# Optimization experiments

Measured on AMD Instinct MI355X. Metric: run time of the kernel, lower is better.

Reference implementation:

```python
import jax, jax.numpy as jnp
import numpy as np

B, I, L = 128, 32, 96   # batch, input_dim, time_series_length
H = 512                  # hidden_dim
F = 24                   # forecast_length (t_eval points)
S = 16                   # n_samples


def _lin(k, out_dim, in_dim):
    kw, kb = jax.random.split(k)
    bound = 1.0 / np.sqrt(in_dim)
    W = jax.random.uniform(kw, (out_dim, in_dim), jnp.float32, -bound, bound)
    b = jax.random.uniform(kb, (out_dim,), jnp.float32, -bound, bound)
    return W, b


def setup_inputs() -> dict:
    key = jax.random.key(0)
    ks = jax.random.split(key, 12)
    enc_Wih, enc_bih = _lin(ks[0], 3 * H, I)
    enc_Whh, enc_bhh = _lin(ks[1], 3 * H, H)
    f_W1, f_b1 = _lin(ks[2], H, H)
    f_W2, f_b2 = _lin(ks[3], H, H)
    g_W, g_b = _lin(ks[4], H, H)
    dec_Wih, dec_bih = _lin(ks[5], 3 * H, H)
    dec_Whh, dec_bhh = _lin(ks[6], 3 * H, H)
    out_W, out_b = _lin(ks[7], I, H)
    x = jax.random.normal(ks[8], (B, I, L), jnp.float32)
    noise = jax.random.normal(ks[9], (S, F - 1, B, H), jnp.float32)  # unit normals -> dW = sqrt(dt)*noise
    return dict(x=x, noise=noise,
                enc_Wih=enc_Wih, enc_Whh=enc_Whh, enc_bih=enc_bih, enc_bhh=enc_bhh,
                f_W1=f_W1, f_b1=f_b1, f_W2=f_W2, f_b2=f_b2,
                g_W=g_W, g_b=g_b,
                dec_Wih=dec_Wih, dec_Whh=dec_Whh, dec_bih=dec_bih, dec_bhh=dec_bhh,
                out_W=out_W, out_b=out_b)


def _gru_cell(gi, gh, h):
    ir, iz, inn = jnp.split(gi, 3, axis=-1)
    hr, hz, hn = jnp.split(gh, 3, axis=-1)
    r = jax.nn.sigmoid(ir + hr)
    z = jax.nn.sigmoid(iz + hz)
    n = jnp.tanh(inn + r * hn)
    return (1.0 - z) * n + z * h


def reference(x, noise, enc_Wih, enc_Whh, enc_bih, enc_bhh,
              f_W1, f_b1, f_W2, f_b2, g_W, g_b,
              dec_Wih, dec_Whh, dec_bih, dec_bhh, out_W, out_b):
    Bb, Ii = x.shape[0], x.shape[1]
    Ss, steps = noise.shape[0], noise.shape[1]
    Hh = enc_Whh.shape[1]
    Ff = steps + 1  # forecast_length; t_eval=linspace(0,F,F) -> F-1 euler steps

    # ---- encoder GRU over [B, L, I] (x permuted from [B, I, L]) ----
    xs = jnp.transpose(x, (0, 2, 1))  # [B, L, I]
    gi_all = jnp.einsum('bli,gi->lbg', xs, enc_Wih) + enc_bih  # [L, B, 3H]

    def enc_step(h, gi):
        gh = h @ enc_Whh.T + enc_bhh
        return _gru_cell(gi, gh, h), None

    h0 = jnp.zeros((Bb, Hh), x.dtype)
    h_enc, _ = jax.lax.scan(enc_step, h0, gi_all)  # [B, H]

    # ---- Euler-Maruyama SDE integration, samples merged into batch ----
    dt = Ff / steps  # linspace(0, F, F): dt = F/(F-1)
    sqdt = jnp.sqrt(jnp.asarray(dt, x.dtype))
    h_sde = jnp.broadcast_to(h_enc, (Ss, Bb, Hh)).reshape(Ss * Bb, Hh)
    dW = (noise * sqdt).transpose(1, 0, 2, 3).reshape(steps, Ss * Bb, Hh)

    def sde_step(h, dw):
        f = jnp.tanh(h @ f_W1.T + f_b1) @ f_W2.T + f_b2
        g = jax.nn.softplus(h @ g_W.T + g_b)
        return h + f * dt + g * dw, None

    h_T, _ = jax.lax.scan(sde_step, h_sde, dW)  # [S*B, H]

    # ---- decoder GRU with zero inputs (input proj reduces to bias) ----
    gi0 = dec_bih  # W_ih @ 0 + b_ih

    def dec_step(h, _):
        gh = h @ dec_Whh.T + dec_bhh
        h_new = _gru_cell(gi0, gh, h)
        return h_new, h_new

    _, hs = jax.lax.scan(dec_step, h_T, None, length=Ff)  # [F, S*B, H]

    out = hs @ out_W.T + out_b          # [F, S*B, I]
    out = out.transpose(1, 2, 0)        # [S*B, I, F]
    return out.reshape(Ss, Bb, Ii, Ff)  # [S, B, I, F]
```

## Files before the change

### kernel.cpp

```cpp
#include <hip/hip_runtime.h>
#include <math.h>

typedef __bf16 bf16x8 __attribute__((ext_vector_type(8)));
typedef float f32x4 __attribute__((ext_vector_type(4)));
typedef unsigned long long u64;

#define HD 512
#define NB 128
#define NI 32
#define NL 96
#define NS 16
#define NF 24
#define NSTEP 23
#define PAD 520

#define MFMA16(a,b,c) __builtin_amdgcn_mfma_f32_16x16x32_bf16(a,b,c,0,0,0)

__device__ __forceinline__ unsigned short f2bf(float f) {
    union { float f; unsigned u; } v; v.f = f;
    unsigned r = v.u + 0x7fffu + ((v.u >> 16) & 1u);
    return (unsigned short)(r >> 16);
}
__device__ __forceinline__ float bf2f(unsigned short h) {
    union { unsigned u; float f; } v; v.u = ((unsigned)h) << 16;
    return v.f;
}
__device__ __forceinline__ void split_bf(float v, unsigned short& hi, unsigned short& lo) {
    unsigned short h = f2bf(v);
    hi = h;
    lo = f2bf(v - bf2f(h));
}
__device__ __forceinline__ float sigm(float x) { return 1.0f / (1.0f + __expf(-x)); }
__device__ __forceinline__ float softp(float x) {
    return fmaxf(x, 0.0f) + log1pf(__expf(-fabsf(x)));
}
__device__ __forceinline__ bf16x8 ld8(const unsigned short* p) {
    return *reinterpret_cast<const bf16x8*>(p);
}
__device__ __forceinline__ f32x4 mfma3(bf16x8 ahi, bf16x8 alo, const unsigned short* bp, f32x4 c) {
    bf16x8 bhi = ld8(bp);
    bf16x8 blo = ld8(bp + 8);
    c = MFMA16(ahi, bhi, c);
    c = MFMA16(alo, bhi, c);
    c = MFMA16(ahi, blo, c);
    return c;
}

__device__ __forceinline__ void sigval(unsigned* slot, unsigned val, int tid) {
    __builtin_amdgcn_s_waitcnt(0);
    __syncthreads();
    if (tid == 0)
        __hip_atomic_store(slot, val, __ATOMIC_RELAXED, __HIP_MEMORY_SCOPE_AGENT);
}
__device__ __forceinline__ void poll8(const unsigned* f, unsigned tgt, int wv, int lane) {
    if (wv == 0) {
        for (;;) {
            unsigned v = __hip_atomic_load(f + (lane & 7), __ATOMIC_RELAXED, __HIP_MEMORY_SCOPE_AGENT);
            if (__all((int)(v >= tgt))) break;
            __builtin_amdgcn_s_sleep(2);
        }
    }
    __syncthreads();
}
__device__ __forceinline__ void stage64(const u64* sh, const u64* sl, int r0,
        unsigned short (*Ahi)[16][PAD], unsigned short (*Alo)[16][PAD], int tid) {
    #pragma unroll 1
    for (int c = 0; c < 4; ++c) {
        u64 th[4], tl[4];
        #pragma unroll
        for (int k = 0; k < 4; ++k) {
            int idx = (c * 4 + k) * 512 + tid;
            int r = idx >> 7, c4 = idx & 127;
            th[k] = __hip_atomic_load(sh + (size_t)(r0 + r) * 128 + c4,
                                      __ATOMIC_RELAXED, __HIP_MEMORY_SCOPE_AGENT);
            tl[k] = __hip_atomic_load(sl + (size_t)(r0 + r) * 128 + c4,
                                      __ATOMIC_RELAXED, __HIP_MEMORY_SCOPE_AGENT);
        }
        #pragma unroll
        for (int k = 0; k < 4; ++k) {
            int idx = (c * 4 + k) * 512 + tid;
            int r = idx >> 7, c4 = idx & 127;
            *(u64*)&Ahi[r >> 4][r & 15][c4 * 4] = th[k];
            *(u64*)&Alo[r >> 4][r & 15][c4 * 4] = tl[k];
        }
    }
}
__device__ __forceinline__ void publish64(u64* dh, u64* dl, int r0, int u0c,
        unsigned short (*Bhi)[72], unsigned short (*Blo)[72], int tid) {
    #pragma unroll
    for (int rep = 0; rep < 4; ++rep) {
        int idx = rep * 512 + tid;
        int pl = idx >> 10, e = idx & 1023;
        int r = e >> 4, c = e & 15;
        u64 q = pl ? *(const u64*)&Blo[r][c * 4] : *(const u64*)&Bhi[r][c * 4];
        u64* dst = (pl ? dl : dh) + (size_t)(r0 + r) * 128 + u0c + c;
        __hip_atomic_store(dst, q, __ATOMIC_RELAXED, __HIP_MEMORY_SCOPE_AGENT);
    }
}

__global__ void pack_w(const float* __restrict__ W, unsigned short* __restrict__ Wp,
                       int N, int K) {
    int idx = blockIdx.x * 256 + threadIdx.x;
    int total = (N / 16) * (K / 32) * 64;
    if (idx >= total) return;
    int lane = idx & 63;
    int t2 = idx >> 6;
    int KT = K / 32;
    int kt = t2 % KT, nt = t2 / KT;
    const float* src = W + (size_t)(nt * 16 + (lane & 15)) * K + kt * 32 + (lane >> 4) * 8;
    unsigned short* dst = Wp + (size_t)idx * 16;
    #pragma unroll
    for (int j = 0; j < 8; ++j) split_bf(src[j], dst[j], dst[8 + j]);
}

__global__ void pack_x(const float* __restrict__ x, unsigned short* __restrict__ xhi,
                       unsigned short* __restrict__ xlo) {
    int idx = blockIdx.x * 256 + threadIdx.x;
    if (idx >= NL * NB) return;
    int b = idx % NB, l = idx / NB;
    size_t base = (size_t)(l * NB + b) * NI;
    #pragma unroll
    for (int i = 0; i < NI; ++i)
        split_bf(x[((size_t)b * NI + i) * NL + l], xhi[base + i], xlo[base + i]);
}

__global__ __launch_bounds__(512, 2) void coop_all(
    const unsigned short* __restrict__ xhi, const unsigned short* __restrict__ xlo,
    const unsigned short* __restrict__ wih_p, const unsigned short* __restrict__ whh_p,
    const unsigned short* __restrict__ w1_p, const unsigned short* __restrict__ w2_p,
    const unsigned short* __restrict__ gw_p, const unsigned short* __restrict__ dwhh_p,
    const unsigned short* __restrict__ outw_p,
    const float* __restrict__ ebih, const float* __restrict__ ebhh,
    const float* __restrict__ fb1, const float* __restrict__ fb2,
    const float* __restrict__ gb, const float* __restrict__ dbih,
    const float* __restrict__ dbhh, const float* __restrict__ outb,
    const float* __restrict__ noise,
    u64* hS0h, u64* hS0l, u64* hS1h, u64* hS1l,
    u64* uPh, u64* uPl, u64* hD0h, u64* hD0l, u64* hD1h, u64* hD1l,
    float* out, unsigned* bar)
{
    const int bid = blockIdx.x;
    const int tid = threadIdx.x, lane = tid & 63, wv = tid >> 6;
    const int l15 = lane & 15, g4 = lane >> 4;
    const f32x4 zz = {0.f, 0.f, 0.f, 0.f};

    __shared__ __align__(16) unsigned char SM[151552];
    auto hA64hi = reinterpret_cast<unsigned short (*)[16][PAD]>(SM);
    auto hA64lo = reinterpret_cast<unsigned short (*)[16][PAD]>(SM + 66560);
    auto uShi   = reinterpret_cast<unsigned short (*)[72]>(SM + 133120);
    auto uSlo   = reinterpret_cast<unsigned short (*)[72]>(SM + 142336);
    auto pred   = reinterpret_cast<float (*)[8][16][16]>(SM);
    auto ehAhi  = reinterpret_cast<unsigned short (*)[PAD]>(SM + 32768);
    auto ehAlo  = reinterpret_cast<unsigned short (*)[PAD]>(SM + 49408);
    auto Shi    = reinterpret_cast<unsigned short (*)[16]>(SM + 66048);
    auto Slo    = reinterpret_cast<unsigned short (*)[16]>(SM + 66560);

    u64* bufh[2] = {hS0h, hS1h};
    u64* bufl[2] = {hS0l, hS1l};

    {
        const int m = bid >> 5, n = bid & 31;
        unsigned* fl = bar + m * 32;
        float cr = 0.f, cz = 0.f, binx = 0.f, bhnn = 0.f, hcell = 0.f;
        const int crow = tid >> 4, cunit = tid & 15;
        if (tid < 256) {
            int u = n * 16 + cunit;
            cr = ebih[u] + ebhh[u];
            cz = ebih[HD + u] + ebhh[HD + u];
            binx = ebih[2 * HD + u];
            bhnn = ebhh[2 * HD + u];
        }
        #pragma unroll 1
        for (int l = 0; l < NL; ++l) {
            bf16x8 axh, axl;
            if (wv == 0) {
                size_t xb = ((size_t)l * NB + m * 16 + l15) * NI + g4 * 8;
                axh = ld8(xhi + xb);
                axl = ld8(xlo + xb);
            }
            if (l > 0) {
                if (wv == 0) {
                    for (;;) {
                        unsigned v = __hip_atomic_load(fl + (lane & 31),
                                     __ATOMIC_RELAXED, __HIP_MEMORY_SCOPE_AGENT);
                        if (__all((int)(v >= (unsigned)l))) break;
                        __builtin_amdgcn_s_sleep(2);
                    }
                }
                __syncthreads();
            }
            {
                const u64* sh = bufh[l & 1];
                const u64* sl = bufl[l & 1];
                u64 qh[4], ql[4];
                #pragma unroll
                for (int rep = 0; rep < 4; ++rep) {
                    int idx = rep * 512 + tid;
                    int r = idx >> 7, c4 = idx & 127;
                    qh[rep] = __hip_atomic_load(sh + (size_t)(m * 16 + r) * 128 + c4,
                                                __ATOMIC_RELAXED, __HIP_MEMORY_SCOPE_AGENT);
                    ql[rep] = __hip_atomic_load(sl + (size_t)(m * 16 + r) * 128 + c4,
                                                __ATOMIC_RELAXED, __HIP_MEMORY_SCOPE_AGENT);
                }
                #pragma unroll
                for (int rep = 0; rep < 4; ++rep) {
                    int idx = rep * 512 + tid;
                    int r = idx >> 7, c4 = idx & 127;
                    *(u64*)&ehAhi[r][c4 * 4] = qh[rep];
                    *(u64*)&ehAlo[r][c4 * 4] = ql[rep];
                }
            }
            __syncthreads();
            f32x4 pr = zz, pz = zz, pnh = zz, pnx = zz;
            if (wv == 0) {
                pr  = mfma3(axh, axl, wih_p + ((size_t)(0 * 32 + n) * 64 + lane) * 16, pr);
                pz  = mfma3(axh, axl, wih_p + ((size_t)(1 * 32 + n) * 64 + lane) * 16, pz);
                pnx = mfma3(axh, axl, wih_p + ((size_t)(2 * 32 + n) * 64 + lane) * 16, pnx);
            }
            #pragma unroll
            for (int kk = 0; kk < 2; ++kk) {
                int kt = wv * 2 + kk;
                bf16x8 ah = *(const bf16x8*)&ehAhi[l15][kt * 32 + g4 * 8];
                bf16x8 al = *(const bf16x8*)&ehAlo[l15][kt * 32 + g4 * 8];
                pr  = mfma3(ah, al, whh_p + ((size_t)((0 * 32 + n) * 16 + kt) * 64 + lane) * 16, pr);
                pz  = mfma3(ah, al, whh_p + ((size_t)((1 * 32 + n) * 16 + kt) * 64 + lane) * 16, pz);
                pnh = mfma3(ah, al, whh_p + ((size_t)((2 * 32 + n) * 16 + kt) * 64 + lane) * 16, pnh);
            }
            #pragma unroll
            for (int v = 0; v < 4; ++v) {
                pred[0][wv][g4 * 4 + v][l15] = pr[v];
                pred[1][wv][g4 * 4 + v][l15] = pz[v];
                pred[2][wv][g4 * 4 + v][l15] = pnh[v];
                if (wv == 0) pred[3][0][g4 * 4 + v][l15] = pnx[v];
            }
            __syncthreads();
            if (tid < 256) {
                float ar = 0.f, az = 0.f, anh_ = 0.f;
                #pragma unroll
                for (int w = 0; w < 8; ++w) {
                    ar += pred[0][w][crow][cunit];
                    az += pred[1][w][crow][cunit];
                    anh_ += pred[2][w][crow][cunit];
                }
                float anx_ = pred[3][0][crow][cunit];
                float r = sigm(ar + cr);
                float z = sigm(az + cz);
                float nn = tanhf(anx_ + binx + r * (anh_ + bhnn));
                hcell = (1.f - z) * nn + z * hcell;
                unsigned short hi, lo;
                split_bf(hcell, hi, lo);
                Shi[crow][cunit] = hi;
                Slo[crow][cunit] = lo;
            }
            __syncthreads();
            if (tid < 128) {
                int p = tid >> 6, t = tid & 63;
                int r = t >> 2, c4 = t & 3;
                u64 q = p ? *(const u64*)&Slo[r][c4 * 4] : *(const u64*)&Shi[r][c4 * 4];
                u64* dst = p ? bufl[(l + 1) & 1] : bufh[(l + 1) & 1];
                __hip_atomic_store(dst + (size_t)(m * 16 + r) * 128 + n * 4 + c4, q,
                                   __ATOMIC_RELAXED, __HIP_MEMORY_SCOPE_AGENT);
            }
            __builtin_amdgcn_s_waitcnt(0);
            __syncthreads();
            if (tid == 0)
                __hip_atomic_store(fl + n, (unsigned)(l + 1),
                                   __ATOMIC_RELAXED, __HIP_MEMORY_SCOPE_AGENT);
        }
        if (tid == 0)
            __hip_atomic_fetch_add(bar + 256, 1u, __ATOMIC_RELAXED, __HIP_MEMORY_SCOPE_AGENT);
    }

    if (tid == 0) {
        while (__hip_atomic_load(bar + 256, __ATOMIC_RELAXED, __HIP_MEMORY_SCOPE_AGENT) < 256u)
            __builtin_amdgcn_s_sleep(2);
    }
    __syncthreads();

    const int m2 = bid >> 3, n2 = bid & 7;
    const int rt = wv & 3, nc = wv >> 2;
    const int r0g = m2 * 64;
    const int u0 = n2 * 64, u0c = n2 * 16;
    const int s = m2 >> 1, b0 = (m2 & 1) * 64;
    unsigned* uf = bar + 320 + m2 * 8;
    unsigned* hf = bar + 576 + m2 * 8;
    u64* hDh[2] = {hD0h, hD1h};
    u64* hDl[2] = {hD0l, hD1l};

    stage64(hS0h, hS0l, b0, hA64hi, hA64lo, tid);
    __syncthreads();

    float hreg[2][4];
    #pragma unroll
    for (int nt = 0; nt < 2; ++nt)
        #pragma unroll
        for (int v = 0; v < 4; ++v) {
            int cc = u0 + nc * 32 + nt * 16 + l15;
            hreg[nt][v] = bf2f(hA64hi[rt][g4 * 4 + v][cc]) + bf2f(hA64lo[rt][g4 * 4 + v][cc]);
        }

    float b1v[2], b2v[2], gbv[2];
    #pragma unroll
    for (int nt = 0; nt < 2; ++nt) {
        int u = u0 + nc * 32 + nt * 16 + l15;
        b1v[nt] = fb1[u]; b2v[nt] = fb2[u]; gbv[nt] = gb[u];
    }
    const float dt = (float)NF / (float)NSTEP;
    const float sqdt = sqrtf(dt);

    #pragma unroll 1
    for (int st = 0; st < NSTEP; ++st) {
        f32x4 au[2] = {zz, zz}, ag[2] = {zz, zz};
        #pragma unroll 2
        for (int kt = 0; kt < 16; ++kt) {
            bf16x8 ah = *(const bf16x8*)&hA64hi[rt][l15][kt * 32 + g4 * 8];
            bf16x8 al = *(const bf16x8*)&hA64lo[rt][l15][kt * 32 + g4 * 8];
            #pragma unroll
            for (int nt = 0; nt < 2; ++nt) {
                int ntg = n2 * 4 + nc * 2 + nt;
                au[nt] = mfma3(ah, al, w1_p + ((size_t)(ntg * 16 + kt) * 64 + lane) * 16, au[nt]);
                ag[nt] = mfma3(ah, al, gw_p + ((size_t)(ntg * 16 + kt) * 64 + lane) * 16, ag[nt]);
            }
        }
        float nz[2][4];
        #pragma unroll
        for (int nt = 0; nt < 2; ++nt)
            #pragma unroll
            for (int v = 0; v < 4; ++v)
                nz[nt][v] = noise[((size_t)(s * NSTEP + st) * NB + b0 + rt * 16 + g4 * 4 + v) * HD
                                  + u0 + nc * 32 + nt * 16 + l15];
        #pragma unroll
        for (int nt = 0; nt < 2; ++nt)
            #pragma unroll
            for (int v = 0; v < 4; ++v) {
                unsigned short hi, lo;
                split_bf(tanhf(au[nt][v] + b1v[nt]), hi, lo);
                uShi[rt * 16 + g4 * 4 + v][nc * 32 + nt * 16 + l15] = hi;
                uSlo[rt * 16 + g4 * 4 + v][nc * 32 + nt * 16 + l15] = lo;
            }
        __syncthreads();
        publish64(uPh, uPl, r0g, u0c, uShi, uSlo, tid);
        sigval(uf + n2, (unsigned)(st + 1), tid);
        poll8(uf, (unsigned)(st + 1), wv, lane);
        stage64(uPh, uPl, r0g, hA64hi, hA64lo, tid);
        __syncthreads();
        f32x4 af[2] = {zz, zz};
        #pragma unroll 2
        for (int kt = 0; kt < 16; ++kt) {
            bf16x8 uh = *(const bf16x8*)&hA64hi[rt][l15][kt * 32 + g4 * 8];
            bf16x8 ul = *(const bf16x8*)&hA64lo[rt][l15][kt * 32 + g4 * 8];
            #pragma unroll
            for (int nt = 0; nt < 2; ++nt) {
                int ntg = n2 * 4 + nc * 2 + nt;
                af[nt] = mfma3(uh, ul, w2_p + ((size_t)(ntg * 16 + kt) * 64 + lane) * 16, af[nt]);
            }
        }
        #pragma unroll
        for (int nt = 0; nt < 2; ++nt)
            #pragma unroll
            for (int v = 0; v < 4; ++v) {
                float gg = softp(ag[nt][v] + gbv[nt]);
                hreg[nt][v] += (af[nt][v] + b2v[nt]) * dt + gg * sqdt * nz[nt][v];
                unsigned short hi, lo;
                split_bf(hreg[nt][v], hi, lo);
                uShi[rt * 16 + g4 * 4 + v][nc * 32 + nt * 16 + l15] = hi;
                uSlo[rt * 16 + g4 * 4 + v][nc * 32 + nt * 16 + l15] = lo;
            }
        __syncthreads();
        publish64(hDh[(st + 1) & 1], hDl[(st + 1) & 1], r0g, u0c, uShi, uSlo, tid);
        sigval(hf + n2, (unsigned)(st + 1), tid);
        poll8(hf, (unsigned)(st + 1), wv, lane);
        stage64(hDh[(st + 1) & 1], hDl[(st + 1) & 1], r0g, hA64hi, hA64lo, tid);
        __syncthreads();
    }

    float crv[2], czv[2], binv[2], bhnv[2];
    #pragma unroll
    for (int nt = 0; nt < 2; ++nt) {
        int u = u0 + nc * 32 + nt * 16 + l15;
        crv[nt] = dbih[u] + dbhh[u];
        czv[nt] = dbih[HD + u] + dbhh[HD + u];
        binv[nt] = dbih[2 * HD + u];
        bhnv[nt] = dbhh[2 * HD + u];
    }
    float obias[2] = {0.f, 0.f};
    if (n2 == 0 && wv < 4) {
        obias[0] = outb[l15];
        obias[1] = outb[16 + l15];
    }

    #pragma unroll 1
    for (int j = 0; j <= NF; ++j) {
        if (j >= 1 && n2 == 0 && wv < 4) {
            f32x4 ao[2] = {zz, zz};
            #pragma unroll 2
            for (int kt = 0; kt < 16; ++kt) {
                bf16x8 ah = *(const bf16x8*)&hA64hi[rt][l15][kt * 32 + g4 * 8];
                bf16x8 al = *(const bf16x8*)&hA64lo[rt][l15][kt * 32 + g4 * 8];
                #pragma unroll
                for (int nt = 0; nt < 2; ++nt)
                    ao[nt] = mfma3(ah, al, outw_p + ((size_t)(nt * 16 + kt) * 64 + lane) * 16, ao[nt]);
            }
            #pragma unroll
            for (int nt = 0; nt < 2; ++nt)
                #pragma unroll
                for (int v = 0; v < 4; ++v) {
                    int b = b0 + rt * 16 + g4 * 4 + v;
                    out[(((size_t)s * NB + b) * NI + nt * 16 + l15) * NF + (j - 1)]
                        = ao[nt][v] + obias[nt];
                }
        }
        if (j == NF) break;
        f32x4 ar[2] = {zz, zz}, az[2] = {zz, zz}, anh[2] = {zz, zz};
        #pragma unroll 2
        for (int kt = 0; kt < 16; ++kt) {
            bf16x8 ah = *(const bf16x8*)&hA64hi[rt][l15][kt * 32 + g4 * 8];
            bf16x8 al = *(const bf16x8*)&hA64lo[rt][l15][kt * 32 + g4 * 8];
            #pragma unroll
            for (int nt = 0; nt < 2; ++nt) {
                int ntg = n2 * 4 + nc * 2 + nt;
                ar[nt]  = mfma3(ah, al, dwhh_p + ((size_t)((ntg) * 16 + kt) * 64 + lane) * 16, ar[nt]);
                az[nt]  = mfma3(ah, al, dwhh_p + ((size_t)((32 + ntg) * 16 + kt) * 64 + lane) * 16, az[nt]);
                anh[nt] = mfma3(ah, al, dwhh_p + ((size_t)((64 + ntg) * 16 + kt) * 64 + lane) * 16, anh[nt]);
            }
        }
        #pragma unroll
        for (int nt = 0; nt < 2; ++nt)
            #pragma unroll
            for (int v = 0; v < 4; ++v) {
                float r = sigm(ar[nt][v] + crv[nt]);
                float z = sigm(az[nt][v] + czv[nt]);
                float nn2 = tanhf(binv[nt] + r * (anh[nt][v] + bhnv[nt]));
                hreg[nt][v] = (1.f - z) * nn2 + z * hreg[nt][v];
                unsigned short hi, lo;
                split_bf(hreg[nt][v], hi, lo);
                uShi[rt * 16 + g4 * 4 + v][nc * 32 + nt * 16 + l15] = hi;
                uSlo[rt * 16 + g4 * 4 + v][nc * 32 + nt * 16 + l15] = lo;
            }
        __syncthreads();
        publish64(hDh[(NSTEP + j + 1) & 1], hDl[(NSTEP + j + 1) & 1], r0g, u0c, uShi, uSlo, tid);
        sigval(hf + n2, (unsigned)(NSTEP + j + 1), tid);
        poll8(hf, (unsigned)(NSTEP + j + 1), wv, lane);
        stage64(hDh[(NSTEP + j + 1) & 1], hDl[(NSTEP + j + 1) & 1], r0g, hA64hi, hA64lo, tid);
        __syncthreads();
    }
}

extern "C" void kernel_launch(void* const* d_in, const int* in_sizes, int n_in,
                              void* d_out, int out_size, void* d_ws, size_t ws_size,
                              hipStream_t stream) {
    const float* x       = (const float*)d_in[0];
    const float* noise   = (const float*)d_in[1];
    const float* enc_Wih = (const float*)d_in[2];
    const float* enc_Whh = (const float*)d_in[3];
    const float* enc_bih = (const float*)d_in[4];
    const float* enc_bhh = (const float*)d_in[5];
    const float* f_W1    = (const float*)d_in[6];
    const float* f_b1    = (const float*)d_in[7];
    const float* f_W2    = (const float*)d_in[8];
    const float* f_b2    = (const float*)d_in[9];
    const float* g_W     = (const float*)d_in[10];
    const float* g_b     = (const float*)d_in[11];
    const float* dec_Whh = (const float*)d_in[13];
    const float* dec_bih = (const float*)d_in[14];
    const float* dec_bhh = (const float*)d_in[15];
    const float* out_W   = (const float*)d_in[16];
    const float* out_b   = (const float*)d_in[17];
    float* out = (float*)d_out;

    char* ws = (char*)d_ws;
    unsigned short* whh_p  = (unsigned short*)(ws + 0);
    unsigned short* wih_p  = (unsigned short*)(ws + 3145728);
    unsigned short* w1_p   = (unsigned short*)(ws + 3342336);
    unsigned short* w2_p   = (unsigned short*)(ws + 4390912);
    unsigned short* gw_p   = (unsigned short*)(ws + 5439488);
    unsigned short* dwhh_p = (unsigned short*)(ws + 6488064);
    unsigned short* outw_p = (unsigned short*)(ws + 9633792);
    unsigned short* xhi    = (unsigned short*)(ws + 9699328);
    unsigned short* xlo    = (unsigned short*)(ws + 10485760);
    u64*            hS0h   = (u64*)(ws + 11272192);
    u64*            hS0l   = (u64*)(ws + 11403264);
    u64*            hS1h   = (u64*)(ws + 11534336);
    u64*            hS1l   = (u64*)(ws + 11665408);
    unsigned*       bar    = (unsigned*)(ws + 11796480);
    u64*            uPh    = (u64*)(ws + 11800576);
    u64*            uPl    = (u64*)(ws + 13897728);
    u64*            hD0h   = (u64*)(ws + 15994880);
    u64*            hD0l   = (u64*)(ws + 18092032);
    u64*            hD1h   = (u64*)(ws + 20189184);
    u64*            hD1l   = (u64*)(ws + 22286336);

    hipMemsetAsync(ws + 11272192, 0, 262144, stream);
    hipMemsetAsync(ws + 11796480, 0, 4096, stream);

    pack_w<<<384, 256, 0, stream>>>(enc_Whh, whh_p, 3 * HD, HD);
    pack_w<<<24, 256, 0, stream>>>(enc_Wih, wih_p, 3 * HD, NI);
    pack_w<<<128, 256, 0, stream>>>(f_W1, w1_p, HD, HD);
    pack_w<<<128, 256, 0, stream>>>(f_W2, w2_p, HD, HD);
    pack_w<<<128, 256, 0, stream>>>(g_W, gw_p, HD, HD);
    pack_w<<<384, 256, 0, stream>>>(dec_Whh, dwhh_p, 3 * HD, HD);
    pack_w<<<8, 256, 0, stream>>>(out_W, outw_p, NI, HD);
    pack_x<<<48, 256, 0, stream>>>(x, xhi, xlo);

    void* args[] = {
        (void*)&xhi, (void*)&xlo, (void*)&wih_p, (void*)&whh_p,
        (void*)&w1_p, (void*)&w2_p, (void*)&gw_p, (void*)&dwhh_p, (void*)&outw_p,
        (void*)&enc_bih, (void*)&enc_bhh, (void*)&f_b1, (void*)&f_b2,
        (void*)&g_b, (void*)&dec_bih, (void*)&dec_bhh, (void*)&out_b,
        (void*)&noise,
        (void*)&hS0h, (void*)&hS0l, (void*)&hS1h, (void*)&hS1l,
        (void*)&uPh, (void*)&uPl, (void*)&hD0h, (void*)&hD0l, (void*)&hD1h, (void*)&hD1l,
        (void*)&out, (void*)&bar
    };
    hipLaunchCooperativeKernel((void*)coop_all, dim3(256), dim3(512), args, 0, stream);
}
```

Before: 1.862 ms.

## Retile SDE/decoder phases to 32-row x 128-unit blocks with 16-byte coherent loads

Changes the per-block tile in the SDE and decoder phases from 64 rows x 64 units to 32 rows x 128 units. Each group of 4 blocks now synchronises instead of 8, and each block stages half as many hidden-state rows, so it also needs less LDS. Global staging loads move from 8-byte atomic loads to inline-asm dwordx4 loads with sc0 sc1 cache bypass, followed by an explicit vmcnt wait. This is meant to cut cross-block traffic and per-step synchronisation cost. The trade-offs are more weight reads per block and a reliance on asm cache bits for coherence.

```diff
diff --git a/kernel.cpp b/kernel.cpp
--- a/kernel.cpp
+++ b/kernel.cpp
@@ -3,6 +3,7 @@
 
 typedef __bf16 bf16x8 __attribute__((ext_vector_type(8)));
 typedef float f32x4 __attribute__((ext_vector_type(4)));
+typedef unsigned int u32x4 __attribute__((ext_vector_type(4)));
 typedef unsigned long long u64;
 
 #define HD 512
@@ -46,52 +47,57 @@
     return c;
 }
 
+__device__ __forceinline__ void ld16i(const void* p, u32x4& d) {
+    asm volatile("global_load_dwordx4 %0, %1, off sc0 sc1"
+                 : "=&v"(d) : "v"(p) : "memory");
+}
+__device__ __forceinline__ void ldfence() {
+    asm volatile("s_waitcnt vmcnt(0)" ::: "memory");
+    __builtin_amdgcn_sched_barrier(0);
+}
+
 __device__ __forceinline__ void sigval(unsigned* slot, unsigned val, int tid) {
     __builtin_amdgcn_s_waitcnt(0);
     __syncthreads();
     if (tid == 0)
         __hip_atomic_store(slot, val, __ATOMIC_RELAXED, __HIP_MEMORY_SCOPE_AGENT);
 }
-__device__ __forceinline__ void poll8(const unsigned* f, unsigned tgt, int wv, int lane) {
+__device__ __forceinline__ void poll4(const unsigned* f, unsigned tgt, int wv, int lane) {
     if (wv == 0) {
         for (;;) {
-            unsigned v = __hip_atomic_load(f + (lane & 7), __ATOMIC_RELAXED, __HIP_MEMORY_SCOPE_AGENT);
+            unsigned v = __hip_atomic_load(f + (lane & 3), __ATOMIC_RELAXED, __HIP_MEMORY_SCOPE_AGENT);
             if (__all((int)(v >= tgt))) break;
             __builtin_amdgcn_s_sleep(2);
         }
     }
     __syncthreads();
 }
-__device__ __forceinline__ void stage64(const u64* sh, const u64* sl, int r0,
+__device__ __forceinline__ void stage32(const u64* sh, const u64* sl, int r0,
         unsigned short (*Ahi)[16][PAD], unsigned short (*Alo)[16][PAD], int tid) {
-    #pragma unroll 1
-    for (int c = 0; c < 4; ++c) {
-        u64 th[4], tl[4];
-        #pragma unroll
-        for (int k = 0; k < 4; ++k) {
-            int idx = (c * 4 + k) * 512 + tid;
-            int r = idx >> 7, c4 = idx & 127;
-            th[k] = __hip_atomic_load(sh + (size_t)(r0 + r) * 128 + c4,
-                                      __ATOMIC_RELAXED, __HIP_MEMORY_SCOPE_AGENT);
-            tl[k] = __hip_atomic_load(sl + (size_t)(r0 + r) * 128 + c4,
-                                      __ATOMIC_RELAXED, __HIP_MEMORY_SCOPE_AGENT);
-        }
-        #pragma unroll
-        for (int k = 0; k < 4; ++k) {
-            int idx = (c * 4 + k) * 512 + tid;
-            int r = idx >> 7, c4 = idx & 127;
-            *(u64*)&Ahi[r >> 4][r & 15][c4 * 4] = th[k];
-            *(u64*)&Alo[r >> 4][r & 15][c4 * 4] = tl[k];
-        }
-    }
-}
-__device__ __forceinline__ void publish64(u64* dh, u64* dl, int r0, int u0c,
-        unsigned short (*Bhi)[72], unsigned short (*Blo)[72], int tid) {
+    u32x4 th[4], tl[4];
+    #pragma unroll
+    for (int k = 0; k < 4; ++k) {
+        int idx = k * 512 + tid;
+        int r = idx >> 6, c8 = idx & 63;
+        ld16i(sh + (size_t)(r0 + r) * 128 + c8 * 2, th[k]);
+        ld16i(sl + (size_t)(r0 + r) * 128 + c8 * 2, tl[k]);
+    }
+    ldfence();
+    #pragma unroll
+    for (int k = 0; k < 4; ++k) {
+        int idx = k * 512 + tid;
+        int r = idx >> 6, c8 = idx & 63;
+        *(u32x4*)&Ahi[r >> 4][r & 15][c8 * 8] = th[k];
+        *(u32x4*)&Alo[r >> 4][r & 15][c8 * 8] = tl[k];
+    }
+}
+__device__ __forceinline__ void publish32(u64* dh, u64* dl, int r0, int u0c,
+        unsigned short (*Bhi)[136], unsigned short (*Blo)[136], int tid) {
     #pragma unroll
     for (int rep = 0; rep < 4; ++rep) {
         int idx = rep * 512 + tid;
         int pl = idx >> 10, e = idx & 1023;
-        int r = e >> 4, c = e & 15;
+        int r = e >> 5, c = e & 31;
         u64 q = pl ? *(const u64*)&Blo[r][c * 4] : *(const u64*)&Bhi[r][c * 4];
         u64* dst = (pl ? dl : dh) + (size_t)(r0 + r) * 128 + u0c + c;
         __hip_atomic_store(dst, q, __ATOMIC_RELAXED, __HIP_MEMORY_SCOPE_AGENT);
@@ -144,11 +150,11 @@
     const int l15 = lane & 15, g4 = lane >> 4;
     const f32x4 zz = {0.f, 0.f, 0.f, 0.f};
 
-    __shared__ __align__(16) unsigned char SM[151552];
-    auto hA64hi = reinterpret_cast<unsigned short (*)[16][PAD]>(SM);
-    auto hA64lo = reinterpret_cast<unsigned short (*)[16][PAD]>(SM + 66560);
-    auto uShi   = reinterpret_cast<unsigned short (*)[72]>(SM + 133120);
-    auto uSlo   = reinterpret_cast<unsigned short (*)[72]>(SM + 142336);
+    __shared__ __align__(16) unsigned char SM[83968];
+    auto hA32hi = reinterpret_cast<unsigned short (*)[16][PAD]>(SM);
+    auto hA32lo = reinterpret_cast<unsigned short (*)[16][PAD]>(SM + 33280);
+    auto uShi   = reinterpret_cast<unsigned short (*)[136]>(SM + 66560);
+    auto uSlo   = reinterpret_cast<unsigned short (*)[136]>(SM + 75264);
     auto pred   = reinterpret_cast<float (*)[8][16][16]>(SM);
     auto ehAhi  = reinterpret_cast<unsigned short (*)[PAD]>(SM + 32768);
     auto ehAlo  = reinterpret_cast<unsigned short (*)[PAD]>(SM + 49408);
@@ -192,22 +198,21 @@
             {
                 const u64* sh = bufh[l & 1];
                 const u64* sl = bufl[l & 1];
-                u64 qh[4], ql[4];
+                u32x4 qh[2], ql[2];
                 #pragma unroll
-                for (int rep = 0; rep < 4; ++rep) {
+                for (int rep = 0; rep < 2; ++rep) {
                     int idx = rep * 512 + tid;
-                    int r = idx >> 7, c4 = idx & 127;
-                    qh[rep] = __hip_atomic_load(sh + (size_t)(m * 16 + r) * 128 + c4,
-                                                __ATOMIC_RELAXED, __HIP_MEMORY_SCOPE_AGENT);
-                    ql[rep] = __hip_atomic_load(sl + (size_t)(m * 16 + r) * 128 + c4,
-                                                __ATOMIC_RELAXED, __HIP_MEMORY_SCOPE_AGENT);
+                    int r = idx >> 6, c8 = idx & 63;
+                    ld16i(sh + (size_t)(m * 16 + r) * 128 + c8 * 2, qh[rep]);
+                    ld16i(sl + (size_t)(m * 16 + r) * 128 + c8 * 2, ql[rep]);
                 }
+                ldfence();
                 #pragma unroll
-                for (int rep = 0; rep < 4; ++rep) {
+                for (int rep = 0; rep < 2; ++rep) {
                     int idx = rep * 512 + tid;
-                    int r = idx >> 7, c4 = idx & 127;
-                    *(u64*)&ehAhi[r][c4 * 4] = qh[rep];
-                    *(u64*)&ehAlo[r][c4 * 4] = ql[rep];
+                    int r = idx >> 6, c8 = idx & 63;
+                    *(u32x4*)&ehAhi[r][c8 * 8] = qh[rep];
+                    *(u32x4*)&ehAlo[r][c8 * 8] = ql[rep];
                 }
             }
             __syncthreads();
@@ -277,17 +282,17 @@
     }
     __syncthreads();
 
-    const int m2 = bid >> 3, n2 = bid & 7;
-    const int rt = wv & 3, nc = wv >> 2;
-    const int r0g = m2 * 64;
-    const int u0 = n2 * 64, u0c = n2 * 16;
-    const int s = m2 >> 1, b0 = (m2 & 1) * 64;
-    unsigned* uf = bar + 320 + m2 * 8;
-    unsigned* hf = bar + 576 + m2 * 8;
+    const int m2 = bid >> 2, n2 = bid & 3;
+    const int rt = wv & 1, nc = wv >> 1;
+    const int r0g = m2 * 32;
+    const int u0 = n2 * 128, u0c = n2 * 32;
+    const int s = m2 >> 2, b0 = (m2 & 3) * 32;
+    unsigned* uf = bar + 320 + m2 * 4;
+    unsigned* hf = bar + 576 + m2 * 4;
     u64* hDh[2] = {hD0h, hD1h};
     u64* hDl[2] = {hD0l, hD1l};
 
-    stage64(hS0h, hS0l, b0, hA64hi, hA64lo, tid);
+    stage32(hS0h, hS0l, b0, hA32hi, hA32lo, tid);
     __syncthreads();
 
     float hreg[2][4];
@@ -296,7 +301,7 @@
         #pragma unroll
         for (int v = 0; v < 4; ++v) {
             int cc = u0 + nc * 32 + nt * 16 + l15;
-            hreg[nt][v] = bf2f(hA64hi[rt][g4 * 4 + v][cc]) + bf2f(hA64lo[rt][g4 * 4 + v][cc]);
+            hreg[nt][v] = bf2f(hA32hi[rt][g4 * 4 + v][cc]) + bf2f(hA32lo[rt][g4 * 4 + v][cc]);
         }
 
     float b1v[2], b2v[2], gbv[2];
@@ -313,11 +318,11 @@
         f32x4 au[2] = {zz, zz}, ag[2] = {zz, zz};
         #pragma unroll 2
         for (int kt = 0; kt < 16; ++kt) {
-            bf16x8 ah = *(const bf16x8*)&hA64hi[rt][l15][kt * 32 + g4 * 8];
-            bf16x8 al = *(const bf16x8*)&hA64lo[rt][l15][kt * 32 + g4 * 8];
+            bf16x8 ah = *(const bf16x8*)&hA32hi[rt][l15][kt * 32 + g4 * 8];
+            bf16x8 al = *(const bf16x8*)&hA32lo[rt][l15][kt * 32 + g4 * 8];
             #pragma unroll
             for (int nt = 0; nt < 2; ++nt) {
-                int ntg = n2 * 4 + nc * 2 + nt;
+                int ntg = n2 * 8 + nc * 2 + nt;
                 au[nt] = mfma3(ah, al, w1_p + ((size_t)(ntg * 16 + kt) * 64 + lane) * 16, au[nt]);
                 ag[nt] = mfma3(ah, al, gw_p + ((size_t)(ntg * 16 + kt) * 64 + lane) * 16, ag[nt]);
             }
@@ -339,19 +344,19 @@
                 uSlo[rt * 16 + g4 * 4 + v][nc * 32 + nt * 16 + l15] = lo;
             }
         __syncthreads();
-        publish64(uPh, uPl, r0g, u0c, uShi, uSlo, tid);
+        publish32(uPh, uPl, r0g, u0c, uShi, uSlo, tid);
         sigval(uf + n2, (unsigned)(st + 1), tid);
-        poll8(uf, (unsigned)(st + 1), wv, lane);
-        stage64(uPh, uPl, r0g, hA64hi, hA64lo, tid);
+        poll4(uf, (unsigned)(st + 1), wv, lane);
+        stage32(uPh, uPl, r0g, hA32hi, hA32lo, tid);
         __syncthreads();
         f32x4 af[2] = {zz, zz};
         #pragma unroll 2
         for (int kt = 0; kt < 16; ++kt) {
-            bf16x8 uh = *(const bf16x8*)&hA64hi[rt][l15][kt * 32 + g4 * 8];
-            bf16x8 ul = *(const bf16x8*)&hA64lo[rt][l15][kt * 32 + g4 * 8];
+            bf16x8 uh = *(const bf16x8*)&hA32hi[rt][l15][kt * 32 + g4 * 8];
+            bf16x8 ul = *(const bf16x8*)&hA32lo[rt][l15][kt * 32 + g4 * 8];
             #pragma unroll
             for (int nt = 0; nt < 2; ++nt) {
-                int ntg = n2 * 4 + nc * 2 + nt;
+                int ntg = n2 * 8 + nc * 2 + nt;
                 af[nt] = mfma3(uh, ul, w2_p + ((size_t)(ntg * 16 + kt) * 64 + lane) * 16, af[nt]);
             }
         }
@@ -367,10 +372,10 @@
                 uSlo[rt * 16 + g4 * 4 + v][nc * 32 + nt * 16 + l15] = lo;
             }
         __syncthreads();
-        publish64(hDh[(st + 1) & 1], hDl[(st + 1) & 1], r0g, u0c, uShi, uSlo, tid);
+        publish32(hDh[(st + 1) & 1], hDl[(st + 1) & 1], r0g, u0c, uShi, uSlo, tid);
         sigval(hf + n2, (unsigned)(st + 1), tid);
-        poll8(hf, (unsigned)(st + 1), wv, lane);
-        stage64(hDh[(st + 1) & 1], hDl[(st + 1) & 1], r0g, hA64hi, hA64lo, tid);
+        poll4(hf, (unsigned)(st + 1), wv, lane);
+        stage32(hDh[(st + 1) & 1], hDl[(st + 1) & 1], r0g, hA32hi, hA32lo, tid);
         __syncthreads();
     }
 
@@ -384,19 +389,19 @@
         bhnv[nt] = dbhh[2 * HD + u];
     }
     float obias[2] = {0.f, 0.f};
-    if (n2 == 0 && wv < 4) {
+    if (n2 == 0 && nc == 0) {
         obias[0] = outb[l15];
         obias[1] = outb[16 + l15];
     }
 
     #pragma unroll 1
     for (int j = 0; j <= NF; ++j) {
-        if (j >= 1 && n2 == 0 && wv < 4) {
+        if (j >= 1 && n2 == 0 && nc == 0) {
             f32x4 ao[2] = {zz, zz};
             #pragma unroll 2
             for (int kt = 0; kt < 16; ++kt) {
-                bf16x8 ah = *(const bf16x8*)&hA64hi[rt][l15][kt * 32 + g4 * 8];
-                bf16x8 al = *(const bf16x8*)&hA64lo[rt][l15][kt * 32 + g4 * 8];
+                bf16x8 ah = *(const bf16x8*)&hA32hi[rt][l15][kt * 32 + g4 * 8];
+                bf16x8 al = *(const bf16x8*)&hA32lo[rt][l15][kt * 32 + g4 * 8];
                 #pragma unroll
                 for (int nt = 0; nt < 2; ++nt)
                     ao[nt] = mfma3(ah, al, outw_p + ((size_t)(nt * 16 + kt) * 64 + lane) * 16, ao[nt]);
@@ -414,11 +419,11 @@
         f32x4 ar[2] = {zz, zz}, az[2] = {zz, zz}, anh[2] = {zz, zz};
         #pragma unroll 2
         for (int kt = 0; kt < 16; ++kt) {
-            bf16x8 ah = *(const bf16x8*)&hA64hi[rt][l15][kt * 32 + g4 * 8];
-            bf16x8 al = *(const bf16x8*)&hA64lo[rt][l15][kt * 32 + g4 * 8];
+            bf16x8 ah = *(const bf16x8*)&hA32hi[rt][l15][kt * 32 + g4 * 8];
+            bf16x8 al = *(const bf16x8*)&hA32lo[rt][l15][kt * 32 + g4 * 8];
             #pragma unroll
             for (int nt = 0; nt < 2; ++nt) {
-                int ntg = n2 * 4 + nc * 2 + nt;
+                int ntg = n2 * 8 + nc * 2 + nt;
                 ar[nt]  = mfma3(ah, al, dwhh_p + ((size_t)((ntg) * 16 + kt) * 64 + lane) * 16, ar[nt]);
                 az[nt]  = mfma3(ah, al, dwhh_p + ((size_t)((32 + ntg) * 16 + kt) * 64 + lane) * 16, az[nt]);
                 anh[nt] = mfma3(ah, al, dwhh_p + ((size_t)((64 + ntg) * 16 + kt) * 64 + lane) * 16, anh[nt]);
@@ -438,10 +443,10 @@
                 uSlo[rt * 16 + g4 * 4 + v][nc * 32 + nt * 16 + l15] = lo;
             }
         __syncthreads();
-        publish64(hDh[(NSTEP + j + 1) & 1], hDl[(NSTEP + j + 1) & 1], r0g, u0c, uShi, uSlo, tid);
+        publish32(hDh[(NSTEP + j + 1) & 1], hDl[(NSTEP + j + 1) & 1], r0g, u0c, uShi, uSlo, tid);
         sigval(hf + n2, (unsigned)(NSTEP + j + 1), tid);
-        poll8(hf, (unsigned)(NSTEP + j + 1), wv, lane);
-        stage64(hDh[(NSTEP + j + 1) & 1], hDl[(NSTEP + j + 1) & 1], r0g, hA64hi, hA64lo, tid);
+        poll4(hf, (unsigned)(NSTEP + j + 1), wv, lane);
+        stage32(hDh[(NSTEP + j + 1) & 1], hDl[(NSTEP + j + 1) & 1], r0g, hA32hi, hA32lo, tid);
         __syncthreads();
     }
 }
```

After: 1.715 ms. 1.09x faster.
